# Performance work log

Hardware: AMD Instinct MI355X
Metric: run time of the kernel (lower is better)

Reference implementation:

```python
import jax, jax.numpy as jnp
import numpy as np


def _star_eigvecs(filter_size: int) -> np.ndarray:
    # Normalized Laplacian of a star graph with filter_size-1 leaves, as in the torch module.
    A = np.zeros((filter_size, filter_size))
    A[0, 1:] = 1.0
    A[1:, 0] = 1.0
    D = np.eye(filter_size)
    D[0, 0] = (filter_size - 1) ** (-0.5)
    L = np.eye(filter_size) - D @ A @ D
    _, u = np.linalg.eigh(L)
    return u.astype(np.float32)


def setup_inputs() -> dict:
    key = jax.random.key(0)
    k1, k2, k3, k4 = jax.random.split(key, 4)
    N_table, fdim = 100000, 256
    B = 10000
    filter_size = 32
    num_sample = filter_size - 2  # 30 neighbors per node
    feat_table = jax.random.normal(k1, (N_table, fdim), dtype=jnp.float32)
    neighbor_idx = jax.random.randint(k2, (B, num_sample), 0, N_table, dtype=jnp.int64)
    # Xavier-uniform for (filter_size, 1) params: bound = sqrt(6/(F+1))
    bound = float(np.sqrt(6.0 / (filter_size + 1)))
    weight = jax.random.uniform(k3, (filter_size, 1), jnp.float32, -bound, bound)
    avgweight = jax.random.uniform(k4, (filter_size, 1), jnp.float32, -bound, bound)
    U = jnp.asarray(_star_eigvecs(filter_size))
    return {"feat_table": feat_table, "neighbor_idx": neighbor_idx,
            "weight": weight, "avgweight": avgweight, "U": U}


def reference(feat_table, neighbor_idx, weight, avgweight, U):
    B, S = neighbor_idx.shape          # S = filter_size - 2
    fdim = feat_table.shape[1]
    # Gather neighbor features: [B, S, fdim]
    gathered = feat_table[neighbor_idx]
    # Pad: slot 0 (center) zero, slots 1..S neighbors, last slot zero -> [B, F, fdim]
    z = jnp.zeros((B, 1, fdim), dtype=feat_table.dtype)
    mask1 = jnp.concatenate([z, gathered, z], axis=1)
    X = jnp.transpose(mask1, (0, 2, 1))                 # [B, fdim, F]
    # Spectral filter: (X @ U) * w  @ U^T  @ avgweight
    Y = jnp.einsum('bdf,fg->bdg', X, U) * weight[:, 0]  # [B, fdim, F]
    Z = jnp.einsum('bdg,fg->bdf', Y, U)                 # X U diag(w) U^T
    out = jnp.einsum('bdf,f->bd', Z, avgweight[:, 0])   # [B, fdim]
    return out
```

## Files before the change

kernel.cpp:

```cpp
#include <hip/hip_runtime.h>

#define FS 32
#define NS 30
#define FDIM 256
#define NSLAB 8
#define SLABW 32
#define BPB 64
#define NXCD 8

__global__ __launch_bounds__(256, 5) void stc_slab128_kernel(
    const float* __restrict__ feat,
    const int*   __restrict__ nidx,
    const float* __restrict__ weight,
    const float* __restrict__ avgw,
    const float* __restrict__ U,
    float* __restrict__ out,
    int B)
{
    __shared__ float t_sh[FS];
    __shared__ float c_sh[FS];
    __shared__ int   idx_sh[BPB * NS];
    __shared__ int   sidx_sh[BPB * NS];
    __shared__ float scoef_sh[BPB * NS];

    const int tid   = threadIdx.x;
    const int slab  = blockIdx.x & (NXCD - 1);
    const int chunk = blockIdx.x >> 3;
    const int b0    = chunk * BPB;

    if (tid < FS) {
        float t = 0.f;
        #pragma unroll
        for (int f = 0; f < FS; ++f) t += U[f * FS + tid] * avgw[f];
        t_sh[tid] = t * weight[tid];
    }
    for (int i = tid; i < BPB * NS; i += 256) {
        int g = b0 * NS + i;
        idx_sh[i] = (g < B * NS) ? nidx[g] : 0;
    }
    __syncthreads();
    if (tid < FS) {
        float c = 0.f;
        #pragma unroll
        for (int g = 0; g < FS; ++g) c += U[tid * FS + g] * t_sh[g];
        c_sh[tid] = c;
    }
    __syncthreads();

    for (int j = tid; j < BPB * NS; j += 256) {
        const int bl = j / NS, s = j - bl * NS;
        const int base = bl * NS;
        const int key = idx_sh[base + s];
        int rank = 0;
        #pragma unroll
        for (int m = 0; m < NS; ++m) {
            const int km = idx_sh[base + m];
            rank += (km < key) || (km == key && m < s);
        }
        sidx_sh[base + rank]  = key;
        scoef_sh[base + rank] = c_sh[s + 1];
    }
    __syncthreads();

    const int bl = tid >> 3;
    const int q  = tid & 7;
    const float* fbase = feat + slab * SLABW + q * 4;
    const int s0 = bl * NS;
    const int s1 = (bl + 32) * NS;

    float4 a0 = make_float4(0.f, 0.f, 0.f, 0.f);
    float4 a1 = make_float4(0.f, 0.f, 0.f, 0.f);

    #pragma unroll 6
    for (int s = 0; s < NS; ++s) {
        const int   r0 = sidx_sh[s0 + s];
        const float c0 = scoef_sh[s0 + s];
        const int   r1 = sidx_sh[s1 + s];
        const float c1 = scoef_sh[s1 + s];
        const float4 v0 = *(const float4*)(fbase + (long long)r0 * FDIM);
        const float4 v1 = *(const float4*)(fbase + (long long)r1 * FDIM);
        a0.x += c0 * v0.x;  a0.y += c0 * v0.y;
        a0.z += c0 * v0.z;  a0.w += c0 * v0.w;
        a1.x += c1 * v1.x;  a1.y += c1 * v1.y;
        a1.z += c1 * v1.z;  a1.w += c1 * v1.w;
    }

    const int bA = b0 + bl, bB = b0 + bl + 32;
    if (bA < B) *((float4*)(out + (long long)bA * FDIM + slab * SLABW) + q) = a0;
    if (bB < B) *((float4*)(out + (long long)bB * FDIM + slab * SLABW) + q) = a1;
}

extern "C" void kernel_launch(void* const* d_in, const int* in_sizes, int n_in,
                              void* d_out, int out_size, void* d_ws, size_t ws_size,
                              hipStream_t stream) {
    const float* feat   = (const float*)d_in[0];
    const int*   nidx   = (const int*)d_in[1];
    const float* weight = (const float*)d_in[2];
    const float* avgw   = (const float*)d_in[3];
    const float* U      = (const float*)d_in[4];
    float* out = (float*)d_out;

    const int B = in_sizes[1] / NS;
    const int chunks = (B + BPB - 1) / BPB;
    const int grid = chunks * NXCD;

    stc_slab128_kernel<<<grid, 256, 0, stream>>>(feat, nidx, weight, avgw, U, out, B);
}
```

Baseline: 48.21 us.

## Relayout feature table to slab-major fp16 before gathering neighbors

Adds a pre-pass that converts the full fp32 feature table to fp16 in the workspace, stored slab-major so each slab's rows sit contiguously. The gather kernel then reads half-width 8-byte chunks from this copy and accumulates in fp32. The goal is to halve the bytes moved by the random gather and improve locality within each slab. The cost is a full read of the table and a half-size write on every call, plus fp16 rounding of the inputs. The original fp32 path is kept as a fallback when the workspace is too small.

Measured after the change: 57.50 us. 1.19x slower.

```diff
diff --git a/kernel.cpp b/kernel.cpp
--- a/kernel.cpp
+++ b/kernel.cpp
@@ -1,21 +1,40 @@
 #include <hip/hip_runtime.h>
+#include <hip/hip_fp16.h>
 
 #define FS 32
 #define NS 30
 #define FDIM 256
-#define NSLAB 8
+#define NXCD 8
 #define SLABW 32
+#define SLABH 32
 #define BPB 64
-#define NXCD 8
-
-__global__ __launch_bounds__(256, 5) void stc_slab128_kernel(
-    const float* __restrict__ feat,
+
+__global__ __launch_bounds__(256) void stc_relayout_f16(
+    const float* __restrict__ feat, __half* __restrict__ t16, int nrow)
+{
+    const int wave = threadIdx.x >> 6, lane = threadIdx.x & 63;
+    const int slab = lane >> 3, oct = lane & 7;
+    const int gw0  = blockIdx.x * 4 + wave;
+    const int nw   = gridDim.x * 4;
+    for (int row = gw0; row < nrow; row += nw) {
+        const float4 v = *((const float4*)(feat + (long long)row * FDIM) + lane);
+        __half2 h01 = __floats2half2_rn(v.x, v.y);
+        __half2 h23 = __floats2half2_rn(v.z, v.w);
+        uint2 u;
+        u.x = *reinterpret_cast<unsigned int*>(&h01);
+        u.y = *reinterpret_cast<unsigned int*>(&h23);
+        *(uint2*)(t16 + ((long long)slab * nrow + row) * SLABH + oct * 4) = u;
+    }
+}
+
+__global__ __launch_bounds__(256, 5) void stc_gather_f16(
+    const __half* __restrict__ t16,
     const int*   __restrict__ nidx,
     const float* __restrict__ weight,
     const float* __restrict__ avgw,
     const float* __restrict__ U,
     float* __restrict__ out,
-    int B)
+    int B, int nrow)
 {
     __shared__ float t_sh[FS];
     __shared__ float c_sh[FS];
@@ -62,15 +81,94 @@
     }
     __syncthreads();
 
-    const int bl = tid >> 3;
-    const int q  = tid & 7;
-    const float* fbase = feat + slab * SLABW + q * 4;
+    const int bl = tid >> 3, oct = tid & 3 | (tid & 7 & ~3) ? tid & 7 : tid & 7;
+    const int o  = tid & 7;
+    const __half* fbase = t16 + (long long)slab * nrow * SLABH + o * 4;
     const int s0 = bl * NS;
     const int s1 = (bl + 32) * NS;
 
     float4 a0 = make_float4(0.f, 0.f, 0.f, 0.f);
     float4 a1 = make_float4(0.f, 0.f, 0.f, 0.f);
 
+    #pragma unroll 6
+    for (int s = 0; s < NS; ++s) {
+        const int   r0 = sidx_sh[s0 + s];
+        const float c0 = scoef_sh[s0 + s];
+        const int   r1 = sidx_sh[s1 + s];
+        const float c1 = scoef_sh[s1 + s];
+        float2 raw0 = *(const float2*)(fbase + ((long long)r0 << 5));
+        float2 raw1 = *(const float2*)(fbase + ((long long)r1 << 5));
+        const __half2 h0a = *reinterpret_cast<__half2*>(&raw0.x);
+        const __half2 h0b = *reinterpret_cast<__half2*>(&raw0.y);
+        const __half2 h1a = *reinterpret_cast<__half2*>(&raw1.x);
+        const __half2 h1b = *reinterpret_cast<__half2*>(&raw1.y);
+        const float2 f0a = __half22float2(h0a), f0b = __half22float2(h0b);
+        const float2 f1a = __half22float2(h1a), f1b = __half22float2(h1b);
+        a0.x += c0 * f0a.x;  a0.y += c0 * f0a.y;
+        a0.z += c0 * f0b.x;  a0.w += c0 * f0b.y;
+        a1.x += c1 * f1a.x;  a1.y += c1 * f1a.y;
+        a1.z += c1 * f1b.x;  a1.w += c1 * f1b.y;
+    }
+
+    const int bA = b0 + bl, bB = b0 + bl + 32;
+    if (bA < B) *((float4*)(out + (long long)bA * FDIM + slab * SLABW) + o) = a0;
+    if (bB < B) *((float4*)(out + (long long)bB * FDIM + slab * SLABW) + o) = a1;
+}
+
+__global__ __launch_bounds__(256, 5) void stc_slab128_kernel(
+    const float* __restrict__ feat, const int* __restrict__ nidx,
+    const float* __restrict__ weight, const float* __restrict__ avgw,
+    const float* __restrict__ U, float* __restrict__ out, int B)
+{
+    __shared__ float t_sh[FS];
+    __shared__ float c_sh[FS];
+    __shared__ int   idx_sh[BPB * NS];
+    __shared__ int   sidx_sh[BPB * NS];
+    __shared__ float scoef_sh[BPB * NS];
+
+    const int tid   = threadIdx.x;
+    const int slab  = blockIdx.x & (NXCD - 1);
+    const int chunk = blockIdx.x >> 3;
+    const int b0    = chunk * BPB;
+
+    if (tid < FS) {
+        float t = 0.f;
+        #pragma unroll
+        for (int f = 0; f < FS; ++f) t += U[f * FS + tid] * avgw[f];
+        t_sh[tid] = t * weight[tid];
+    }
+    for (int i = tid; i < BPB * NS; i += 256) {
+        int g = b0 * NS + i;
+        idx_sh[i] = (g < B * NS) ? nidx[g] : 0;
+    }
+    __syncthreads();
+    if (tid < FS) {
+        float c = 0.f;
+        #pragma unroll
+        for (int g = 0; g < FS; ++g) c += U[tid * FS + g] * t_sh[g];
+        c_sh[tid] = c;
+    }
+    __syncthreads();
+    for (int j = tid; j < BPB * NS; j += 256) {
+        const int bl = j / NS, s = j - bl * NS;
+        const int base = bl * NS;
+        const int key = idx_sh[base + s];
+        int rank = 0;
+        #pragma unroll
+        for (int m = 0; m < NS; ++m) {
+            const int km = idx_sh[base + m];
+            rank += (km < key) || (km == key && m < s);
+        }
+        sidx_sh[base + rank]  = key;
+        scoef_sh[base + rank] = c_sh[s + 1];
+    }
+    __syncthreads();
+
+    const int bl = tid >> 3, q = tid & 7;
+    const float* fbase = feat + slab * SLABW + q * 4;
+    const int s0 = bl * NS, s1 = (bl + 32) * NS;
+    float4 a0 = make_float4(0.f, 0.f, 0.f, 0.f);
+    float4 a1 = make_float4(0.f, 0.f, 0.f, 0.f);
     #pragma unroll 6
     for (int s = 0; s < NS; ++s) {
         const int   r0 = sidx_sh[s0 + s];
@@ -84,7 +182,6 @@
         a1.x += c1 * v1.x;  a1.y += c1 * v1.y;
         a1.z += c1 * v1.z;  a1.w += c1 * v1.w;
     }
-
     const int bA = b0 + bl, bB = b0 + bl + 32;
     if (bA < B) *((float4*)(out + (long long)bA * FDIM + slab * SLABW) + q) = a0;
     if (bB < B) *((float4*)(out + (long long)bB * FDIM + slab * SLABW) + q) = a1;
@@ -100,9 +197,17 @@
     const float* U      = (const float*)d_in[4];
     float* out = (float*)d_out;
 
-    const int B = in_sizes[1] / NS;
+    const int B    = in_sizes[1] / NS;
+    const int nrow = in_sizes[0] / FDIM;
     const int chunks = (B + BPB - 1) / BPB;
-    const int grid = chunks * NXCD;
-
-    stc_slab128_kernel<<<grid, 256, 0, stream>>>(feat, nidx, weight, avgw, U, out, B);
-}
+    const int grid   = chunks * NXCD;
+
+    const size_t need = (size_t)NXCD * nrow * SLABH * sizeof(__half);
+    if (ws_size >= need) {
+        __half* t16 = (__half*)d_ws;
+        stc_relayout_f16<<<2048, 256, 0, stream>>>(feat, t16, nrow);
+        stc_gather_f16<<<grid, 256, 0, stream>>>(t16, nidx, weight, avgw, U, out, B, nrow);
+    } else {
+        stc_slab128_kernel<<<grid, 256, 0, stream>>>(feat, nidx, weight, avgw, U, out, B);
+    }
+}
```
